# Performance work log

Hardware: AMD Instinct MI355X
Metric: run time of the kernel (lower is better)

Reference implementation:

```python
import jax, jax.numpy as jnp
import numpy as np

N = 50000   # nodes
E = 800000  # edges (avg degree 16)
D = 2048    # resnet50 feature dim
C = 256     # layer_size
NEG_SLOPE = 0.2


def setup_inputs() -> dict:
    key = jax.random.key(0)
    ks = jax.random.split(key, 16)
    s = 0.02
    inp = {
        'x': jax.random.normal(ks[0], (N, D), jnp.float32),
        'edge_index': jax.random.randint(ks[1], (2, E), 0, N, dtype=jnp.int32),
        # GATConv layer 1 (in=D, out=C, heads=1)
        'W1': jax.random.normal(ks[2], (D, C), jnp.float32) * s,
        'a_src1': jax.random.normal(ks[3], (C,), jnp.float32) * s,
        'a_dst1': jax.random.normal(ks[4], (C,), jnp.float32) * s,
        'b1': jnp.zeros((C,), jnp.float32),
        # GATConv layer 2 (in=C, out=C)
        'W2': jax.random.normal(ks[5], (C, C), jnp.float32) * s,
        'a_src2': jax.random.normal(ks[6], (C,), jnp.float32) * s,
        'a_dst2': jax.random.normal(ks[7], (C,), jnp.float32) * s,
        'b2': jnp.zeros((C,), jnp.float32),
        # EdgePredictor: lin1 (2C -> C), lin2 (C -> 1)
        'Wp1': jax.random.normal(ks[8], (2 * C, C), jnp.float32) * s,
        'bp1': jnp.zeros((C,), jnp.float32),
        'wp2': jax.random.normal(ks[9], (C,), jnp.float32) * s,
        'bp2': jnp.zeros((), jnp.float32),
    }
    return inp


def gat_layer(x, src, dst, W, a_src, a_dst, b, n_nodes):
    # PyG GATConv, heads=1, concat=True: message flows src -> dst,
    # softmax over incoming edges of each dst node.
    h = x @ W                                   # [N, C]
    e = jax.nn.leaky_relu((h @ a_src)[src] + (h @ a_dst)[dst], NEG_SLOPE)  # [E]
    emax = jax.ops.segment_max(e, dst, num_segments=n_nodes)
    ex = jnp.exp(e - emax[dst])
    denom = jax.ops.segment_sum(ex, dst, num_segments=n_nodes)
    alpha = ex / (denom[dst] + 1e-16)           # [E]
    out = jax.ops.segment_sum(h[src] * alpha[:, None], dst, num_segments=n_nodes)
    return out + b


def reference(x, edge_index, W1, a_src1, a_dst1, b1, W2, a_src2, a_dst2, b2,
              Wp1, bp1, wp2, bp2):
    src, dst = edge_index[0], edge_index[1]
    # GATConv default add_self_loops=True
    loops = jnp.arange(N, dtype=src.dtype)
    src_sl = jnp.concatenate([src, loops])
    dst_sl = jnp.concatenate([dst, loops])

    h = gat_layer(x, src_sl, dst_sl, W1, a_src1, a_dst1, b1, N)
    h = gat_layer(h, src_sl, dst_sl, W2, a_src2, a_dst2, b2, N)

    # edge predictor on the ORIGINAL edge_index (no self loops)
    xe = jnp.concatenate([h[src], h[dst]], axis=-1)       # [E, 2C]
    z = jax.nn.relu(xe @ Wp1 + bp1)                        # [E, C]  (dropout: eval mode)
    return z @ wp2 + bp2                                   # [E]
```

## Files before the change

kernel.cpp:

```cpp
#include <hip/hip_runtime.h>
#include <hip/hip_bf16.h>
#include <stdint.h>

#define NNODES 50000
#define NEDGES 800000
#define DIN    2048
#define CDIM   256
#define ELOOP  (NEDGES + NNODES)

using bf16x8 = __attribute__((ext_vector_type(8))) short;
using f32x4  = __attribute__((ext_vector_type(4))) float;
using gvoid  = __attribute__((address_space(1))) const void;
using lvoid  = __attribute__((address_space(3))) void;

__device__ __forceinline__ float bf2f(uint16_t u) {
    union { uint32_t i; float f; } v; v.i = (uint32_t)u << 16; return v.f;
}
__device__ __forceinline__ uint16_t f2bf(float f) {
    union { float f; uint32_t i; } v; v.f = f;
    uint32_t i = v.i;
    return (uint16_t)((i + 0x7FFFu + ((i >> 16) & 1u)) >> 16);
}

#define BM 128
#define BN 128
#define BK 32

#define WAITVM(N) asm volatile("s_waitcnt vmcnt(" #N ")" ::: "memory")

__global__ __launch_bounds__(256)
void gemm_bt(const uint16_t* __restrict__ A, const uint16_t* __restrict__ Bt,
             uint16_t* __restrict__ C, const float* __restrict__ bias,
             int M, int N, int K)
{
    __shared__ __align__(16) uint16_t lA[3][BM * BK];
    __shared__ __align__(16) uint16_t lB[3][BN * BK];
    const int tid  = threadIdx.x;
    const int wave = tid >> 6;
    const int lane = tid & 63;
    const int lm = lane & 15, lq = lane >> 4;
    const int bm = blockIdx.x * BM;
    const int bn = blockIdx.y * BN;
    const int wm = (wave >> 1) * 64;
    const int wn = (wave & 1) * 64;

    f32x4 acc[4][4];
    for (int i = 0; i < 4; ++i)
        for (int j = 0; j < 4; ++j)
            acc[i][j] = (f32x4)0.0f;

    auto stage = [&](int buf, int k0) {
        for (int j = 0; j < 2; ++j) {
            int c = j * 256 + wave * 64 + lane;
            int row = c >> 2, cc = c & 3;
            int gr = bm + row; if (gr >= M) gr = M - 1;
            const uint16_t* gp = A + (size_t)gr * K + k0 + cc * 8;
            __builtin_amdgcn_global_load_lds((gvoid*)gp,
                (lvoid*)(lA[buf] + (size_t)(j * 256 + wave * 64) * 8), 16, 0, 0);
        }
        for (int j = 0; j < 2; ++j) {
            int c = j * 256 + wave * 64 + lane;
            int row = c >> 2, cc = c & 3;
            const uint16_t* gp = Bt + (size_t)(bn + row) * K + k0 + cc * 8;
            __builtin_amdgcn_global_load_lds((gvoid*)gp,
                (lvoid*)(lB[buf] + (size_t)(j * 256 + wave * 64) * 8), 16, 0, 0);
        }
    };

    const int ntiles = K / BK;
    stage(0, 0);
    stage(1, BK);
    WAITVM(4);
    __builtin_amdgcn_s_barrier();

    for (int t = 0; t < ntiles; ++t) {
        const int cur = t % 3;
        if (t + 2 < ntiles) stage((t + 2) % 3, (t + 2) * BK);

        bf16x8 af[4], bfr[4];
        for (int mt = 0; mt < 4; ++mt)
            af[mt] = *(const bf16x8*)(lA[cur] + (wm + mt * 16 + lm) * BK + lq * 8);
        for (int nt2 = 0; nt2 < 4; ++nt2)
            bfr[nt2] = *(const bf16x8*)(lB[cur] + (wn + nt2 * 16 + lm) * BK + lq * 8);

        for (int mt = 0; mt < 4; ++mt)
            for (int nt2 = 0; nt2 < 4; ++nt2)
                acc[mt][nt2] = __builtin_amdgcn_mfma_f32_16x16x32_bf16(
                    af[mt], bfr[nt2], acc[mt][nt2], 0, 0, 0);

        if (t + 1 < ntiles) {
            if (t + 2 < ntiles) WAITVM(4);
            else                WAITVM(0);
            __builtin_amdgcn_s_barrier();
        }
    }

    for (int mt = 0; mt < 4; ++mt) {
        for (int nt2 = 0; nt2 < 4; ++nt2) {
            int gn = bn + wn + nt2 * 16 + lm;
            float badd = bias ? bias[gn] : 0.0f;
            for (int r = 0; r < 4; ++r) {
                int gm = bm + wm + mt * 16 + lq * 4 + r;
                if (gm < M)
                    C[(size_t)gm * N + gn] = f2bf(acc[mt][nt2][r] + badd);
            }
        }
    }
}

__global__ __launch_bounds__(256)
void gemm_f32_bt(const float* __restrict__ A, const uint16_t* __restrict__ Bt,
                 uint16_t* __restrict__ C, int M, int N, int K)
{
    __shared__ __align__(16) float    lA[3][BM * BK];
    __shared__ __align__(16) uint16_t lB[3][BN * BK];
    const int tid  = threadIdx.x;
    const int wave = tid >> 6;
    const int lane = tid & 63;
    const int lm = lane & 15, lq = lane >> 4;
    const int bm = blockIdx.x * BM;
    const int bn = blockIdx.y * BN;
    const int wm = (wave >> 1) * 64;
    const int wn = (wave & 1) * 64;

    f32x4 acc[4][4];
    for (int i = 0; i < 4; ++i)
        for (int j = 0; j < 4; ++j)
            acc[i][j] = (f32x4)0.0f;

    auto stage = [&](int buf, int k0) {
        for (int j = 0; j < 4; ++j) {
            int c = j * 256 + wave * 64 + lane;
            int row = c >> 3;
            int lc  = (c & 7) ^ (row & 7);
            int gr = bm + row; if (gr >= M) gr = M - 1;
            const float* gp = A + (size_t)gr * K + k0 + lc * 4;
            __builtin_amdgcn_global_load_lds((gvoid*)gp,
                (lvoid*)(lA[buf] + (size_t)(j * 256 + wave * 64) * 4), 16, 0, 0);
        }
        for (int j = 0; j < 2; ++j) {
            int c = j * 256 + wave * 64 + lane;
            int row = c >> 2, cc = c & 3;
            const uint16_t* gp = Bt + (size_t)(bn + row) * K + k0 + cc * 8;
            __builtin_amdgcn_global_load_lds((gvoid*)gp,
                (lvoid*)(lB[buf] + (size_t)(j * 256 + wave * 64) * 8), 16, 0, 0);
        }
    };

    const int ntiles = K / BK;
    stage(0, 0);
    stage(1, BK);
    WAITVM(6);
    __builtin_amdgcn_s_barrier();

    for (int t = 0; t < ntiles; ++t) {
        const int cur = t % 3;
        if (t + 2 < ntiles) stage((t + 2) % 3, (t + 2) * BK);

        bf16x8 af[4], bfr[4];
        for (int mt = 0; mt < 4; ++mt) {
            int r = wm + mt * 16 + lm;
            int s0 = (lq * 2)     ^ (r & 7);
            int s1 = (lq * 2 + 1) ^ (r & 7);
            f32x4 a0 = *(const f32x4*)(lA[cur] + r * BK + s0 * 4);
            f32x4 a1 = *(const f32x4*)(lA[cur] + r * BK + s1 * 4);
            bf16x8 t2;
            for (int q = 0; q < 4; ++q) {
                t2[q]     = (short)f2bf(a0[q]);
                t2[q + 4] = (short)f2bf(a1[q]);
            }
            af[mt] = t2;
        }
        for (int nt2 = 0; nt2 < 4; ++nt2)
            bfr[nt2] = *(const bf16x8*)(lB[cur] + (wn + nt2 * 16 + lm) * BK + lq * 8);

        for (int mt = 0; mt < 4; ++mt)
            for (int nt2 = 0; nt2 < 4; ++nt2)
                acc[mt][nt2] = __builtin_amdgcn_mfma_f32_16x16x32_bf16(
                    af[mt], bfr[nt2], acc[mt][nt2], 0, 0, 0);

        if (t + 1 < ntiles) {
            if (t + 2 < ntiles) WAITVM(6);
            else                WAITVM(0);
            __builtin_amdgcn_s_barrier();
        }
    }

    for (int mt = 0; mt < 4; ++mt) {
        for (int nt2 = 0; nt2 < 4; ++nt2) {
            int gn = bn + wn + nt2 * 16 + lm;
            for (int r = 0; r < 4; ++r) {
                int gm = bm + wm + mt * 16 + lq * 4 + r;
                if (gm < M)
                    C[(size_t)gm * N + gn] = f2bf(acc[mt][nt2][r]);
            }
        }
    }
}

__global__ __launch_bounds__(256)
void transpose_cvt_kernel(const float* __restrict__ W,
                          uint16_t* __restrict__ Wt, int K, int N)
{
    __shared__ float tile[32][33];
    const int k0 = blockIdx.x * 32, n0 = blockIdx.y * 32;
    const int tx = threadIdx.x & 31, ty = threadIdx.x >> 5;
    for (int r = 0; r < 32; r += 8)
        tile[ty + r][tx] = W[(size_t)(k0 + ty + r) * N + n0 + tx];
    __syncthreads();
    for (int r = 0; r < 32; r += 8)
        Wt[(size_t)(n0 + ty + r) * K + k0 + tx] = f2bf(tile[tx][ty + r]);
}

__global__ void bias512_kernel(const float* __restrict__ bp1,
                               float* __restrict__ bias512)
{
    int i = blockIdx.x * 256 + threadIdx.x;
    if (i < 512) bias512[i] = (i < 256) ? bp1[i] : 0.0f;
}

__global__ void count_kernel(const int* __restrict__ ei, int* __restrict__ rs)
{
    int i = blockIdx.x * 256 + threadIdx.x;
    if (i >= ELOOP) return;
    int dst = (i < NEDGES) ? ei[NEDGES + i] : (i - NEDGES);
    atomicAdd(&rs[dst + 1], 1);
}

__global__ __launch_bounds__(1024)
void scan_part_kernel(int* __restrict__ rs, int* __restrict__ bsum)
{
    __shared__ int wsum[16];
    const int b = blockIdx.x, tid = threadIdx.x, lane = tid & 63, w = tid >> 6;
    int i = b * 1024 + tid;
    int v = (i <= NNODES) ? rs[i] : 0;
    int s = v;
    for (int d = 1; d < 64; d <<= 1) {
        int t = __shfl_up(s, d);
        if (lane >= d) s += t;
    }
    if (lane == 63) wsum[w] = s;
    __syncthreads();
    if (tid < 16) {
        int x = wsum[tid];
        for (int d = 1; d < 16; d <<= 1) {
            int t = __shfl_up(x, d);
            if (tid >= d) x += t;
        }
        wsum[tid] = x;
    }
    __syncthreads();
    int incl = s + (w > 0 ? wsum[w - 1] : 0);
    if (i <= NNODES) rs[i] = incl;
    if (tid == 1023) bsum[b] = incl;
}

__global__ void scan_bsum_kernel(int* __restrict__ bsum, int nb)
{
    int tid = threadIdx.x;
    int v = (tid < nb) ? bsum[tid] : 0;
    for (int d = 1; d < 64; d <<= 1) {
        int t = __shfl_up(v, d);
        if (tid >= d) v += t;
    }
    if (tid < nb) bsum[tid] = v;
}

__global__ __launch_bounds__(1024)
void scan_add_kernel(const int* __restrict__ bsum, int* __restrict__ rs,
                     int* __restrict__ cursor)
{
    int b = blockIdx.x;
    int i = b * 1024 + threadIdx.x;
    int add = b ? bsum[b - 1] : 0;
    if (i <= NNODES) {
        int r = rs[i] + add;
        rs[i] = r;
        if (i < NNODES) cursor[i] = r;
    }
}

__global__ void fill_kernel(const int* __restrict__ ei, int* __restrict__ cursor,
                            int* __restrict__ csr_src)
{
    int i = blockIdx.x * 256 + threadIdx.x;
    if (i >= ELOOP) return;
    int src, dst;
    if (i < NEDGES) { src = ei[i]; dst = ei[NEDGES + i]; }
    else            { src = dst = i - NEDGES; }
    int pos = atomicAdd(&cursor[dst], 1);
    csr_src[pos] = src;
}

__global__ __launch_bounds__(256)
void rowdot_kernel(const uint16_t* __restrict__ g,
                   const float* __restrict__ asrc,
                   const float* __restrict__ adst,
                   float* __restrict__ s_src, float* __restrict__ s_dst)
{
    int n = blockIdx.x * 4 + (threadIdx.x >> 6);
    int lane = threadIdx.x & 63;
    ushort4 rv = *(const ushort4*)(g + (size_t)n * CDIM + lane * 4);
    float4 av = *(const float4*)(asrc + lane * 4);
    float4 dv = *(const float4*)(adst + lane * 4);
    float r0 = bf2f(rv.x), r1 = bf2f(rv.y), r2 = bf2f(rv.z), r3 = bf2f(rv.w);
    float a = r0 * av.x + r1 * av.y + r2 * av.z + r3 * av.w;
    float b = r0 * dv.x + r1 * dv.y + r2 * dv.z + r3 * dv.w;
    for (int d = 32; d; d >>= 1) { a += __shfl_xor(a, d); b += __shfl_xor(b, d); }
    if (lane == 0) { s_src[n] = a; s_dst[n] = b; }
}

__global__ __launch_bounds__(256)
void attn_kernel(const int* __restrict__ row_start, const int* __restrict__ csr_src,
                 const float* __restrict__ s_src, const float* __restrict__ s_dst,
                 const uint16_t* __restrict__ g, const float* __restrict__ bvec,
                 uint16_t* __restrict__ hout)
{
    int n = blockIdx.x * 4 + (threadIdx.x >> 6);
    int lane = threadIdx.x & 63;
    int h = lane >> 5, hl = lane & 31;
    int beg = row_start[n], end = row_start[n + 1];
    float sdn = s_dst[n];

    float m = -1e30f;
    for (int i = beg + lane; i < end; i += 64) {
        float e = s_src[csr_src[i]] + sdn;
        e = (e > 0.f) ? e : 0.2f * e;
        m = fmaxf(m, e);
    }
    for (int d = 32; d; d >>= 1) m = fmaxf(m, __shfl_xor(m, d));

    float sum = 0.f;
    for (int i = beg + lane; i < end; i += 64) {
        float e = s_src[csr_src[i]] + sdn;
        e = (e > 0.f) ? e : 0.2f * e;
        sum += __expf(e - m);
    }
    for (int d = 32; d; d >>= 1) sum += __shfl_xor(sum, d);
    float inv = 1.f / (sum + 1e-16f);

    float a0 = 0.f, a1 = 0.f, a2 = 0.f, a3 = 0.f;
    float a4 = 0.f, a5 = 0.f, a6 = 0.f, a7 = 0.f;
    for (int i = beg + h; i < end; i += 2) {
        int src = csr_src[i];
        float e = s_src[src] + sdn;
        e = (e > 0.f) ? e : 0.2f * e;
        float alpha = __expf(e - m) * inv;
        uint4 rv = *(const uint4*)(g + (size_t)src * CDIM + hl * 8);
        a0 += alpha * bf2f((uint16_t)(rv.x & 0xffffu));
        a1 += alpha * bf2f((uint16_t)(rv.x >> 16));
        a2 += alpha * bf2f((uint16_t)(rv.y & 0xffffu));
        a3 += alpha * bf2f((uint16_t)(rv.y >> 16));
        a4 += alpha * bf2f((uint16_t)(rv.z & 0xffffu));
        a5 += alpha * bf2f((uint16_t)(rv.z >> 16));
        a6 += alpha * bf2f((uint16_t)(rv.w & 0xffffu));
        a7 += alpha * bf2f((uint16_t)(rv.w >> 16));
    }
    a0 += __shfl_xor(a0, 32); a1 += __shfl_xor(a1, 32);
    a2 += __shfl_xor(a2, 32); a3 += __shfl_xor(a3, 32);
    a4 += __shfl_xor(a4, 32); a5 += __shfl_xor(a5, 32);
    a6 += __shfl_xor(a6, 32); a7 += __shfl_xor(a7, 32);

    if (h == 0) {
        const float4 b0 = *(const float4*)(bvec + hl * 8);
        const float4 b1 = *(const float4*)(bvec + hl * 8 + 4);
        uint4 o;
        o.x = (uint32_t)f2bf(a0 + b0.x) | ((uint32_t)f2bf(a1 + b0.y) << 16);
        o.y = (uint32_t)f2bf(a2 + b0.z) | ((uint32_t)f2bf(a3 + b0.w) << 16);
        o.z = (uint32_t)f2bf(a4 + b1.x) | ((uint32_t)f2bf(a5 + b1.y) << 16);
        o.w = (uint32_t)f2bf(a6 + b1.z) | ((uint32_t)f2bf(a7 + b1.w) << 16);
        *(uint4*)(hout + (size_t)n * CDIM + hl * 8) = o;
    }
}

__global__ __launch_bounds__(256)
void edgepred_kernel(const int* __restrict__ ei,
                     const uint16_t* __restrict__ UV,
                     const float* __restrict__ wp2, const float* __restrict__ bp2,
                     float* __restrict__ out)
{
    const int tid = threadIdx.x;
    const int grp = tid >> 4, l = tid & 15;
    const int e = blockIdx.x * 16 + grp;
    int src = ei[e];
    int dst = ei[NEDGES + e];
    const uint16_t* Up = UV + (size_t)src * 512 + l * 16;
    const uint16_t* Vp = UV + (size_t)dst * 512 + 256 + l * 16;
    const uint4 u0 = *(const uint4*)(Up);
    const uint4 u1 = *(const uint4*)(Up + 8);
    const uint4 v0 = *(const uint4*)(Vp);
    const uint4 v1 = *(const uint4*)(Vp + 8);
    const float4 w0 = *(const float4*)(wp2 + l * 16);
    const float4 w1 = *(const float4*)(wp2 + l * 16 + 4);
    const float4 w2 = *(const float4*)(wp2 + l * 16 + 8);
    const float4 w3 = *(const float4*)(wp2 + l * 16 + 12);
    float acc = 0.f;
    auto proc = [&](uint32_t uu, uint32_t vv, float wa, float wb) {
        float z0 = fmaxf(bf2f((uint16_t)(uu & 0xffffu)) + bf2f((uint16_t)(vv & 0xffffu)), 0.f);
        float z1 = fmaxf(bf2f((uint16_t)(uu >> 16)) + bf2f((uint16_t)(vv >> 16)), 0.f);
        acc += z0 * wa + z1 * wb;
    };
    proc(u0.x, v0.x, w0.x, w0.y); proc(u0.y, v0.y, w0.z, w0.w);
    proc(u0.z, v0.z, w1.x, w1.y); proc(u0.w, v0.w, w1.z, w1.w);
    proc(u1.x, v1.x, w2.x, w2.y); proc(u1.y, v1.y, w2.z, w2.w);
    proc(u1.z, v1.z, w3.x, w3.y); proc(u1.w, v1.w, w3.z, w3.w);
    for (int d = 1; d < 16; d <<= 1) acc += __shfl_xor(acc, d);
    if (l == 0) out[e] = acc + *bp2;
}

extern "C" void kernel_launch(void* const* d_in, const int* in_sizes, int n_in,
                              void* d_out, int out_size, void* d_ws, size_t ws_size,
                              hipStream_t stream)
{
    const float* x   = (const float*)d_in[0];
    const int*   ei  = (const int*)d_in[1];
    const float* W1  = (const float*)d_in[2];
    const float* as1 = (const float*)d_in[3];
    const float* ad1 = (const float*)d_in[4];
    const float* b1  = (const float*)d_in[5];
    const float* W2  = (const float*)d_in[6];
    const float* as2 = (const float*)d_in[7];
    const float* ad2 = (const float*)d_in[8];
    const float* b2  = (const float*)d_in[9];
    const float* Wp1 = (const float*)d_in[10];
    const float* bp1 = (const float*)d_in[11];
    const float* wp2 = (const float*)d_in[12];
    const float* bp2 = (const float*)d_in[13];
    float* out = (float*)d_out;

    char* ws = (char*)d_ws;
    size_t off = 0;
    auto alloc = [&](size_t bytes) -> void* {
        void* p = ws + off;
        off += (bytes + 255) & ~(size_t)255;
        return p;
    };
    uint16_t* W1t   = (uint16_t*)alloc((size_t)DIN * CDIM * 2);
    uint16_t* W2t   = (uint16_t*)alloc((size_t)CDIM * CDIM * 2);
    uint16_t* WpABt = (uint16_t*)alloc((size_t)2 * CDIM * CDIM * 2);
    int* row_start = (int*)alloc((NNODES + 1) * sizeof(int));
    int* cursor    = (int*)alloc(NNODES * sizeof(int));
    int* csr_src   = (int*)alloc((size_t)ELOOP * sizeof(int));
    int* bsum      = (int*)alloc(64 * sizeof(int));
    float* s_src   = (float*)alloc(NNODES * sizeof(float));
    float* s_dst   = (float*)alloc(NNODES * sizeof(float));
    float* bias512 = (float*)alloc(512 * sizeof(float));
    uint16_t* H    = (uint16_t*)alloc((size_t)NNODES * CDIM * 2);
    uint16_t* G    = (uint16_t*)alloc((size_t)NNODES * CDIM * 2);
    uint16_t* Vb   = (uint16_t*)alloc((size_t)NNODES * CDIM * 2);
    (void)Vb;
    uint16_t* UV   = G;

    hipMemsetAsync(row_start, 0, (NNODES + 1) * sizeof(int), stream);

    transpose_cvt_kernel<<<dim3(DIN / 32, CDIM / 32), 256, 0, stream>>>(W1, W1t, DIN, CDIM);
    transpose_cvt_kernel<<<dim3(CDIM / 32, CDIM / 32), 256, 0, stream>>>(W2, W2t, CDIM, CDIM);
    transpose_cvt_kernel<<<dim3(CDIM / 32, CDIM / 32), 256, 0, stream>>>(Wp1, WpABt, CDIM, CDIM);
    transpose_cvt_kernel<<<dim3(CDIM / 32, CDIM / 32), 256, 0, stream>>>(Wp1 + CDIM * CDIM, WpABt + CDIM * CDIM, CDIM, CDIM);
    bias512_kernel<<<2, 256, 0, stream>>>(bp1, bias512);

    const int NB = (NNODES + 1 + 1023) / 1024;
    count_kernel<<<(ELOOP + 255) / 256, 256, 0, stream>>>(ei, row_start);
    scan_part_kernel<<<NB, 1024, 0, stream>>>(row_start, bsum);
    scan_bsum_kernel<<<1, 64, 0, stream>>>(bsum, NB);
    scan_add_kernel<<<NB, 1024, 0, stream>>>(bsum, row_start, cursor);
    fill_kernel<<<(ELOOP + 255) / 256, 256, 0, stream>>>(ei, cursor, csr_src);

    dim3 gg((NNODES + BM - 1) / BM, CDIM / BN);

    gemm_f32_bt<<<gg, 256, 0, stream>>>(x, W1t, G, NNODES, CDIM, DIN);
    rowdot_kernel<<<NNODES / 4, 256, 0, stream>>>(G, as1, ad1, s_src, s_dst);
    attn_kernel<<<NNODES / 4, 256, 0, stream>>>(row_start, csr_src, s_src, s_dst, G, b1, H);

    gemm_bt<<<gg, 256, 0, stream>>>(H, W2t, G, nullptr, NNODES, CDIM, CDIM);
    rowdot_kernel<<<NNODES / 4, 256, 0, stream>>>(G, as2, ad2, s_src, s_dst);
    attn_kernel<<<NNODES / 4, 256, 0, stream>>>(row_start, csr_src, s_src, s_dst, G, b2, H);

    dim3 gg2((NNODES + BM - 1) / BM, 512 / BN);
    gemm_bt<<<gg2, 256, 0, stream>>>(H, WpABt, UV, bias512, NNODES, 512, CDIM);

    edgepred_kernel<<<NEDGES / 16, 256, 0, stream>>>(ei, UV, wp2, bp2, out);
}
```

Baseline: 1.146 ms.

## Fuse attention score row-dots into GEMM epilogues and use packed bf16 convert

The separate rowdot kernels are removed. Each GEMM epilogue now computes the partial dot products of its accumulator tile with a_src and a_dst, reduces them across lanes with shuffles, and adds them into zeroed score buffers with atomics. This drops two launches and two full reads of G, at the cost of extra memsets, float atomics (two column blocks per row) and some epilogue work. The fp32-to-bf16 conversion in the first GEMM also switches to the hardware v_cvt_pk_bf16_f32 instruction instead of manual rounding. Scores now come from fp32 accumulators rather than the bf16-rounded G, which slightly changes numerics.

```diff
diff --git a/kernel.cpp b/kernel.cpp
--- a/kernel.cpp
+++ b/kernel.cpp
@@ -28,9 +28,41 @@
 
 #define WAITVM(N) asm volatile("s_waitcnt vmcnt(" #N ")" ::: "memory")
 
+#define ROWDOT_EPILOGUE()                                                     \
+    if (s_src) {                                                              \
+        float av[4], dv[4];                                                   \
+        for (int nt2 = 0; nt2 < 4; ++nt2) {                                   \
+            int gn = bn + wn + nt2 * 16 + lm;                                 \
+            av[nt2] = asrc[gn];                                               \
+            dv[nt2] = adst[gn];                                               \
+        }                                                                     \
+        for (int mt = 0; mt < 4; ++mt)                                        \
+            for (int r = 0; r < 4; ++r) {                                     \
+                float ps = 0.f, pd = 0.f;                                     \
+                for (int nt2 = 0; nt2 < 4; ++nt2) {                           \
+                    float v = acc[mt][nt2][r];                                \
+                    ps += v * av[nt2];                                        \
+                    pd += v * dv[nt2];                                        \
+                }                                                             \
+                for (int d = 1; d < 16; d <<= 1) {                            \
+                    ps += __shfl_xor(ps, d);                                  \
+                    pd += __shfl_xor(pd, d);                                  \
+                }                                                             \
+                if (lm == 0) {                                                \
+                    int gm = bm + wm + mt * 16 + lq * 4 + r;                  \
+                    if (gm < M) {                                             \
+                        atomicAdd(&s_src[gm], ps);                            \
+                        atomicAdd(&s_dst[gm], pd);                            \
+                    }                                                         \
+                }                                                             \
+            }                                                                 \
+    }
+
 __global__ __launch_bounds__(256)
 void gemm_bt(const uint16_t* __restrict__ A, const uint16_t* __restrict__ Bt,
              uint16_t* __restrict__ C, const float* __restrict__ bias,
+             const float* __restrict__ asrc, const float* __restrict__ adst,
+             float* __restrict__ s_src, float* __restrict__ s_dst,
              int M, int N, int K)
 {
     __shared__ __align__(16) uint16_t lA[3][BM * BK];
@@ -106,11 +138,16 @@
             }
         }
     }
+
+    ROWDOT_EPILOGUE();
 }
 
 __global__ __launch_bounds__(256)
 void gemm_f32_bt(const float* __restrict__ A, const uint16_t* __restrict__ Bt,
-                 uint16_t* __restrict__ C, int M, int N, int K)
+                 uint16_t* __restrict__ C,
+                 const float* __restrict__ asrc, const float* __restrict__ adst,
+                 float* __restrict__ s_src, float* __restrict__ s_dst,
+                 int M, int N, int K)
 {
     __shared__ __align__(16) float    lA[3][BM * BK];
     __shared__ __align__(16) uint16_t lB[3][BN * BK];
@@ -164,12 +201,14 @@
             int s1 = (lq * 2 + 1) ^ (r & 7);
             f32x4 a0 = *(const f32x4*)(lA[cur] + r * BK + s0 * 4);
             f32x4 a1 = *(const f32x4*)(lA[cur] + r * BK + s1 * 4);
-            bf16x8 t2;
-            for (int q = 0; q < 4; ++q) {
-                t2[q]     = (short)f2bf(a0[q]);
-                t2[q + 4] = (short)f2bf(a1[q]);
-            }
-            af[mt] = t2;
+            union { uint32_t u[4]; bf16x8 v; } t2;
+            float x0 = a0[0], x1 = a0[1], x2 = a0[2], x3 = a0[3];
+            float y0 = a1[0], y1 = a1[1], y2 = a1[2], y3 = a1[3];
+            asm("v_cvt_pk_bf16_f32 %0, %1, %2" : "=v"(t2.u[0]) : "v"(x0), "v"(x1));
+            asm("v_cvt_pk_bf16_f32 %0, %1, %2" : "=v"(t2.u[1]) : "v"(x2), "v"(x3));
+            asm("v_cvt_pk_bf16_f32 %0, %1, %2" : "=v"(t2.u[2]) : "v"(y0), "v"(y1));
+            asm("v_cvt_pk_bf16_f32 %0, %1, %2" : "=v"(t2.u[3]) : "v"(y2), "v"(y3));
+            af[mt] = t2.v;
         }
         for (int nt2 = 0; nt2 < 4; ++nt2)
             bfr[nt2] = *(const bf16x8*)(lB[cur] + (wn + nt2 * 16 + lm) * BK + lq * 8);
@@ -196,6 +235,8 @@
             }
         }
     }
+
+    ROWDOT_EPILOGUE();
 }
 
 __global__ __launch_bounds__(256)
@@ -290,24 +331,6 @@
     else            { src = dst = i - NEDGES; }
     int pos = atomicAdd(&cursor[dst], 1);
     csr_src[pos] = src;
-}
-
-__global__ __launch_bounds__(256)
-void rowdot_kernel(const uint16_t* __restrict__ g,
-                   const float* __restrict__ asrc,
-                   const float* __restrict__ adst,
-                   float* __restrict__ s_src, float* __restrict__ s_dst)
-{
-    int n = blockIdx.x * 4 + (threadIdx.x >> 6);
-    int lane = threadIdx.x & 63;
-    ushort4 rv = *(const ushort4*)(g + (size_t)n * CDIM + lane * 4);
-    float4 av = *(const float4*)(asrc + lane * 4);
-    float4 dv = *(const float4*)(adst + lane * 4);
-    float r0 = bf2f(rv.x), r1 = bf2f(rv.y), r2 = bf2f(rv.z), r3 = bf2f(rv.w);
-    float a = r0 * av.x + r1 * av.y + r2 * av.z + r3 * av.w;
-    float b = r0 * dv.x + r1 * dv.y + r2 * dv.z + r3 * dv.w;
-    for (int d = 32; d; d >>= 1) { a += __shfl_xor(a, d); b += __shfl_xor(b, d); }
-    if (lane == 0) { s_src[n] = a; s_dst[n] = b; }
 }
 
 __global__ __launch_bounds__(256)
@@ -442,8 +465,9 @@
     int* cursor    = (int*)alloc(NNODES * sizeof(int));
     int* csr_src   = (int*)alloc((size_t)ELOOP * sizeof(int));
     int* bsum      = (int*)alloc(64 * sizeof(int));
-    float* s_src   = (float*)alloc(NNODES * sizeof(float));
-    float* s_dst   = (float*)alloc(NNODES * sizeof(float));
+    float* sbuf    = (float*)alloc((size_t)2 * NNODES * sizeof(float));
+    float* s_src   = sbuf;
+    float* s_dst   = sbuf + NNODES;
     float* bias512 = (float*)alloc(512 * sizeof(float));
     uint16_t* H    = (uint16_t*)alloc((size_t)NNODES * CDIM * 2);
     uint16_t* G    = (uint16_t*)alloc((size_t)NNODES * CDIM * 2);
@@ -452,6 +476,7 @@
     uint16_t* UV   = G;
 
     hipMemsetAsync(row_start, 0, (NNODES + 1) * sizeof(int), stream);
+    hipMemsetAsync(sbuf, 0, (size_t)2 * NNODES * sizeof(float), stream);
 
     transpose_cvt_kernel<<<dim3(DIN / 32, CDIM / 32), 256, 0, stream>>>(W1, W1t, DIN, CDIM);
     transpose_cvt_kernel<<<dim3(CDIM / 32, CDIM / 32), 256, 0, stream>>>(W2, W2t, CDIM, CDIM);
@@ -468,16 +493,18 @@
 
     dim3 gg((NNODES + BM - 1) / BM, CDIM / BN);
 
-    gemm_f32_bt<<<gg, 256, 0, stream>>>(x, W1t, G, NNODES, CDIM, DIN);
-    rowdot_kernel<<<NNODES / 4, 256, 0, stream>>>(G, as1, ad1, s_src, s_dst);
+    gemm_f32_bt<<<gg, 256, 0, stream>>>(x, W1t, G, as1, ad1, s_src, s_dst,
+                                        NNODES, CDIM, DIN);
     attn_kernel<<<NNODES / 4, 256, 0, stream>>>(row_start, csr_src, s_src, s_dst, G, b1, H);
 
-    gemm_bt<<<gg, 256, 0, stream>>>(H, W2t, G, nullptr, NNODES, CDIM, CDIM);
-    rowdot_kernel<<<NNODES / 4, 256, 0, stream>>>(G, as2, ad2, s_src, s_dst);
+    hipMemsetAsync(sbuf, 0, (size_t)2 * NNODES * sizeof(float), stream);
+    gemm_bt<<<gg, 256, 0, stream>>>(H, W2t, G, nullptr, as2, ad2, s_src, s_dst,
+                                    NNODES, CDIM, CDIM);
     attn_kernel<<<NNODES / 4, 256, 0, stream>>>(row_start, csr_src, s_src, s_dst, G, b2, H);
 
     dim3 gg2((NNODES + BM - 1) / BM, 512 / BN);
-    gemm_bt<<<gg2, 256, 0, stream>>>(H, WpABt, UV, bias512, NNODES, 512, CDIM);
+    gemm_bt<<<gg2, 256, 0, stream>>>(H, WpABt, UV, bias512, nullptr, nullptr,
+                                     nullptr, nullptr, NNODES, 512, CDIM);
 
     edgepred_kernel<<<NEDGES / 16, 256, 0, stream>>>(ei, UV, wp2, bp2, out);
 }
```

Measured after the change: 1.109 ms. -3.2%, faster.
